# Optimization experiments

Measured on AMD Instinct MI355X. Metric: run time of the kernel, lower is better.

Reference implementation:

```python
import jax, jax.numpy as jnp
import numpy as np

D_MODEL, D_HEAD, N_HEAD = 1024, 64, 16
B, T1, T2 = 2, 2048, 2048


def setup_inputs() -> dict:
    key = jax.random.key(0)
    ks = jax.random.split(key, 8)
    s = 1.0 / np.sqrt(D_MODEL)
    return {
        "x": jax.random.normal(ks[0], (B, T1, D_MODEL), dtype=jnp.float32),
        "context": jax.random.normal(ks[1], (B, T2, D_MODEL), dtype=jnp.float32),
        "bias": jax.random.normal(ks[2], (T1, T2), dtype=jnp.float32),
        "W_q": jax.random.normal(ks[3], (D_MODEL, N_HEAD * D_HEAD), dtype=jnp.float32) * s,
        "W_k": jax.random.normal(ks[4], (D_MODEL, N_HEAD * D_HEAD), dtype=jnp.float32) * s,
        "W_v": jax.random.normal(ks[5], (D_MODEL, N_HEAD * D_HEAD), dtype=jnp.float32) * s,
        "W_out": jax.random.normal(ks[6], (N_HEAD * D_HEAD, D_MODEL), dtype=jnp.float32) * s,
        "b_out": jnp.zeros((D_MODEL,), dtype=jnp.float32),
    }


def reference(x, context, bias, W_q, W_k, W_v, W_out, b_out):
    Bq, T1_, _ = x.shape
    T2_ = context.shape[1]
    atten_scale = 1.0 / np.sqrt(D_HEAD)
    # fixed (non-trainable) per-head scale: 2^{-1}, ..., 2^{-n_head}
    head_scale = jnp.exp2(-jnp.arange(1, N_HEAD + 1, dtype=jnp.float32))

    # projections -> [B, H, T, d]
    q = (x @ W_q).reshape(Bq, T1_, N_HEAD, D_HEAD).transpose(0, 2, 1, 3)
    k = (context @ W_k).reshape(Bq, T2_, N_HEAD, D_HEAD).transpose(0, 2, 1, 3)
    v = (context @ W_v).reshape(Bq, T2_, N_HEAD, D_HEAD).transpose(0, 2, 1, 3)

    # scores: [B, H, T1, T2]
    scores = jnp.einsum("bhqd,bhkd->bhqk", q, k) * atten_scale
    scores = scores + bias[None, None, :, :] * head_scale[None, :, None, None]
    attn = jax.nn.softmax(scores, axis=-1)

    out = jnp.einsum("bhqk,bhkd->bqhd", attn, v).reshape(Bq, T1_, N_HEAD * D_HEAD)
    # dropout is identity in eval mode
    return out @ W_out + b_out
```

## Files before the change

### kernel.cpp

```cpp
#include <hip/hip_runtime.h>

typedef float  f32x4   __attribute__((ext_vector_type(4)));
typedef float  f32x16  __attribute__((ext_vector_type(16)));
typedef __bf16 bf16x8  __attribute__((ext_vector_type(8)));
typedef __bf16 bf16x4  __attribute__((ext_vector_type(4)));
typedef __bf16 bf16x2  __attribute__((ext_vector_type(2)));
typedef short  short8v __attribute__((ext_vector_type(8)));
typedef unsigned uint4v __attribute__((ext_vector_type(4)));

__device__ __forceinline__ short f2bf(float f) {
  unsigned u = __float_as_uint(f);
  unsigned r = (u + 0x7FFFu + ((u >> 16) & 1u)) >> 16;
  return (short)r;
}

__device__ __forceinline__ f32x4 mfma16(bf16x8 a, bf16x8 b, f32x4 c) {
  return __builtin_amdgcn_mfma_f32_16x16x32_bf16(a, b, c, 0, 0, 0);
}
__device__ __forceinline__ f32x16 mfma32(bf16x8 a, bf16x8 b, f32x16 c) {
  return __builtin_amdgcn_mfma_f32_32x32x16_bf16(a, b, c, 0, 0, 0);
}

__device__ __forceinline__ void gload16(const void* g, void* l) {
  __builtin_amdgcn_global_load_lds(
      (const __attribute__((address_space(1))) unsigned int*)g,
      (__attribute__((address_space(3))) unsigned int*)l,
      16, 0, 0);
}

__device__ __forceinline__ bf16x8 p_exchange(const unsigned* pk, int a, int hi) {
  unsigned y1 = hi ? pk[4 * a + 0] : pk[4 * a + 2];
  unsigned z1 = __shfl_xor(y1, 32);
  unsigned y2 = hi ? pk[4 * a + 1] : pk[4 * a + 3];
  unsigned z2 = __shfl_xor(y2, 32);
  unsigned w0 = hi ? z1 : pk[4 * a + 0];
  unsigned w1 = hi ? z2 : pk[4 * a + 1];
  unsigned w2 = hi ? pk[4 * a + 2] : z1;
  unsigned w3 = hi ? pk[4 * a + 3] : z2;
  uint4v q4 = {w0, w1, w2, w3};
  return __builtin_bit_cast(bf16x8, q4);
}


__global__ __launch_bounds__(256) void cvt_copy(const float* __restrict__ in,
                                                short* __restrict__ out, int n4) {
  int i = blockIdx.x * blockDim.x + threadIdx.x;
  int stride = gridDim.x * blockDim.x;
  for (; i < n4; i += stride) {
    float4 v = *(const float4*)&in[i * 4];
    short4 o;
    o.x = f2bf(v.x); o.y = f2bf(v.y); o.z = f2bf(v.z); o.w = f2bf(v.w);
    *(short4*)&out[i * 4] = o;
  }
}

__global__ __launch_bounds__(256) void cvt_transpose4(const float* __restrict__ W0,
                                                      const float* __restrict__ W1,
                                                      const float* __restrict__ W2,
                                                      const float* __restrict__ W3,
                                                      short* __restrict__ T0,
                                                      short* __restrict__ T1,
                                                      short* __restrict__ T2,
                                                      short* __restrict__ T3) {
  __shared__ short t_s[64][72];
  int z = blockIdx.z;
  const float* W = (z == 0) ? W0 : (z == 1) ? W1 : (z == 2) ? W2 : W3;
  short* Wt = (z == 0) ? T0 : (z == 1) ? T1 : (z == 2) ? T2 : T3;
  int k0 = blockIdx.y * 64, n0 = blockIdx.x * 64;
  int tid = threadIdx.x;
#pragma unroll
  for (int i = 0; i < 4; i++) {
    int idx = i * 256 + tid;
    int r = idx >> 4, cg = idx & 15;
    float4 v = *(const float4*)&W[(k0 + r) * 1024 + n0 + cg * 4];
    t_s[cg * 4 + 0][r] = f2bf(v.x);
    t_s[cg * 4 + 1][r] = f2bf(v.y);
    t_s[cg * 4 + 2][r] = f2bf(v.z);
    t_s[cg * 4 + 3][r] = f2bf(v.w);
  }
  __syncthreads();
#pragma unroll
  for (int i = 0; i < 2; i++) {
    int idx = i * 256 + tid;
    int r = idx >> 3, cg = idx & 7;
    short8v val = *(short8v*)&t_s[r][cg * 8];
    *(short8v*)&Wt[(n0 + r) * 1024 + k0 + cg * 8] = val;
  }
}

template <int EPI>
__global__ __launch_bounds__(256, 4) void gemm_bf16(const short* __restrict__ A,
                                                    const short* __restrict__ Bt,
                                                    void* __restrict__ out,
                                                    void* __restrict__ out2,
                                                    const float* __restrict__ bout) {
  constexpr int KD = 1024;
  constexpr int NB = (EPI == 3) ? 32 : 16;
  __shared__ short a_s[64][64];
  __shared__ short b_s[64][64];
  int tid = threadIdx.x, w = tid >> 6, lane = tid & 63;
  int g = lane >> 4, c16 = lane & 15;
  int hsw = c16 & 7;

  int lin = blockIdx.x + NB * blockIdx.y;
  int wk = (lin & 7) * (NB * 8) + (lin >> 3);
  int c0 = (wk & (NB - 1)) * 64, r0 = (wk / NB) * 64;

  int wr = (w >> 1) * 32, wc = (w & 1) * 32;
  f32x4 acc[2][2] = {};

  for (int kt = 0; kt < KD / 64; ++kt) {
    int k0 = kt * 64;
    __syncthreads();
#pragma unroll
    for (int i = 0; i < 2; i++) {
      int cb = i * 256 + w * 64;
      int c = cb + lane;
      int row = c >> 3, kg = c & 7;
      int sw = (kg ^ (row & 7)) * 8;
      gload16(A + (r0 + row) * KD + k0 + sw, (char*)a_s + cb * 16);
      gload16(Bt + (c0 + row) * KD + k0 + sw, (char*)b_s + cb * 16);
    }
    __syncthreads();
#pragma unroll
    for (int kk = 0; kk < 2; kk++) {
      bf16x8 af[2], bf[2];
      int sl0 = ((4 * kk + g) ^ hsw) * 8;
#pragma unroll
      for (int m = 0; m < 2; m++) af[m] = *(const bf16x8*)&a_s[wr + m * 16 + c16][sl0];
#pragma unroll
      for (int n = 0; n < 2; n++) bf[n] = *(const bf16x8*)&b_s[wc + n * 16 + c16][sl0];
#pragma unroll
      for (int m = 0; m < 2; m++)
#pragma unroll
        for (int n = 0; n < 2; n++) acc[m][n] = mfma16(af[m], bf[n], acc[m][n]);
    }
  }

#pragma unroll
  for (int m = 0; m < 2; m++)
#pragma unroll
    for (int n = 0; n < 2; n++)
#pragma unroll
      for (int r = 0; r < 4; r++) {
        int row = r0 + wr + m * 16 + g * 4 + r;
        int col = c0 + wc + n * 16 + c16;
        float v = acc[m][n][r];
        int b = row >> 11, t = row & 2047;
        if (EPI == 2) {
          ((float*)out)[row * 1024 + col] = v + bout[col];
        } else if (EPI == 0) {
          int h = col >> 6, d = col & 63;
          ((short*)out)[(((b * 16 + h) * 2048) + t) * 64 + d] = f2bf(v);
        } else {
          if (col < 1024) {
            int h = col >> 6, d = col & 63;
            ((short*)out)[(((b * 16 + h) * 2048) + t) * 64 + d] = f2bf(v);
          } else {
            int cv = col - 1024;
            int h = cv >> 6, d = cv & 63;
            ((short*)out2)[(((b * 16 + h) * 64) + d) * 2048 + t] = f2bf(v);
          }
        }
      }
}

__global__ __launch_bounds__(256, 4) void flash_attn(const short* __restrict__ Qg,
                                                     const short* __restrict__ Kg,
                                                     const short* __restrict__ Vtg,
                                                     const short* __restrict__ biasb,
                                                     short* __restrict__ Og) {
  __shared__ short k_s[2][64][64];
  __shared__ short v_s[2][64][64];

  int tid = threadIdx.x, w = tid >> 6, lane = tid & 63;
  int hi = lane >> 5, ll = lane & 31;
  int l7 = ll & 7;

  int lin = blockIdx.x + 16 * (blockIdx.y + 16 * blockIdx.z);
  int qi = (lin & 7) | (((lin >> 8) & 1) << 3);
  int h = (lin >> 3) & 15;
  int b = (lin >> 7) & 1;
  int qb = qi * 128;

  const short* Qh = Qg + (size_t)(b * 16 + h) * 2048 * 64;
  const short* Kh = Kg + (size_t)(b * 16 + h) * 2048 * 64;
  const short* Vh = Vtg + (size_t)(b * 16 + h) * 64 * 2048;

  const float C1 = 0.125f * 1.44269504f;
  const float C2 = exp2f(-(float)(h + 1)) * 1.44269504f;

  int qrow = qb + w * 32 + ll;
  const short* bp = biasb + (size_t)qrow * 2048 + 4 * hi;

#pragma unroll
  for (int i = 0; i < 2; i++) {
    int cb = i * 256 + w * 64;
    int c = cb + lane;
    int row = c >> 3, t8 = c & 7, sw = (t8 ^ (row & 7)) * 8;
    gload16(Kh + row * 64 + sw, (char*)&k_s[0][0][0] + cb * 16);
    gload16(Vh + row * 2048 + sw, (char*)&v_s[0][0][0] + cb * 16);
  }
  bf16x8 qf[4];
#pragma unroll
  for (int dm = 0; dm < 4; dm++)
    qf[dm] = *(const bf16x8*)(Qh + (size_t)qrow * 64 + dm * 16 + hi * 8);
  asm volatile("" ::: "memory");

  float l_run = 0.f;
  f32x16 o_acc[2] = {};

  for (int kt = 0; kt < 32; ++kt) {
    int cur = kt & 1;
    bf16x4 bv0[4];
#pragma unroll
    for (int u = 0; u < 4; u++)
      bv0[u] = *(const bf16x4*)(bp + kt * 64 + u * 8);

    if (kt < 31) {
      const short* Ks = Kh + (size_t)(kt + 1) * 64 * 64;
      const short* Vs = Vh + (kt + 1) * 64;
#pragma unroll
      for (int i = 0; i < 2; i++) {
        int cb = i * 256 + w * 64;
        int c = cb + lane;
        int row = c >> 3, t8 = c & 7, sw = (t8 ^ (row & 7)) * 8;
        gload16(Ks + row * 64 + sw, (char*)&k_s[cur ^ 1][0][0] + cb * 16);
        gload16(Vs + row * 2048 + sw, (char*)&v_s[cur ^ 1][0][0] + cb * 16);
      }
    }
    asm volatile("s_waitcnt vmcnt(8)" ::: "memory");
    __builtin_amdgcn_s_barrier();

    f32x16 sacc = {};
    __builtin_amdgcn_s_setprio(1);
#pragma unroll
    for (int dm = 0; dm < 4; dm++) {
      const short* kr = &k_s[cur][ll][((2 * dm + hi) ^ l7) * 8];
      sacc = mfma32(*(const bf16x8*)kr, qf[dm], sacc);
    }
    __builtin_amdgcn_s_setprio(0);

    float lp = 0.f;
    unsigned pk[8];
#pragma unroll
    for (int i = 0; i < 8; i++) {
      float b0 = (float)bv0[i >> 1][2 * (i & 1)];
      float b1 = (float)bv0[i >> 1][2 * (i & 1) + 1];
      float p0 = exp2f(sacc[2 * i] * C1 + b0 * C2);
      float p1 = exp2f(sacc[2 * i + 1] * C1 + b1 * C2);
      lp += p0 + p1;
      bf16x2 pp = {(__bf16)p0, (__bf16)p1};
      pk[i] = __builtin_bit_cast(unsigned, pp);
    }
    l_run += lp;

    bf16x4 bv1[4];
#pragma unroll
    for (int u = 0; u < 4; u++)
      bv1[u] = *(const bf16x4*)(bp + kt * 64 + 32 + u * 8);

    __builtin_amdgcn_s_setprio(1);
#pragma unroll
    for (int a = 0; a < 2; a++) {
      bf16x8 PA = p_exchange(pk, a, hi);
#pragma unroll
      for (int dt = 0; dt < 2; dt++) {
        const short* vr = &v_s[cur][dt * 32 + ll][((2 * a + hi) ^ l7) * 8];
        o_acc[dt] = mfma32(PA, *(const bf16x8*)vr, o_acc[dt]);
      }
    }
    __builtin_amdgcn_s_setprio(0);
    asm volatile("" ::: "memory");

    f32x16 sacc1 = {};
    __builtin_amdgcn_s_setprio(1);
#pragma unroll
    for (int dm = 0; dm < 4; dm++) {
      const short* kr = &k_s[cur][32 + ll][((2 * dm + hi) ^ l7) * 8];
      sacc1 = mfma32(*(const bf16x8*)kr, qf[dm], sacc1);
    }
    __builtin_amdgcn_s_setprio(0);

    float lp1 = 0.f;
#pragma unroll
    for (int i = 0; i < 8; i++) {
      float b0 = (float)bv1[i >> 1][2 * (i & 1)];
      float b1 = (float)bv1[i >> 1][2 * (i & 1) + 1];
      float p0 = exp2f(sacc1[2 * i] * C1 + b0 * C2);
      float p1 = exp2f(sacc1[2 * i + 1] * C1 + b1 * C2);
      lp1 += p0 + p1;
      bf16x2 pp = {(__bf16)p0, (__bf16)p1};
      pk[i] = __builtin_bit_cast(unsigned, pp);
    }
    l_run += lp1;

    __builtin_amdgcn_s_setprio(1);
#pragma unroll
    for (int a = 0; a < 2; a++) {
      bf16x8 PA = p_exchange(pk, a, hi);
#pragma unroll
      for (int dt = 0; dt < 2; dt++) {
        const short* vr = &v_s[cur][dt * 32 + ll][((4 + 2 * a + hi) ^ l7) * 8];
        o_acc[dt] = mfma32(PA, *(const bf16x8*)vr, o_acc[dt]);
      }
    }
    __builtin_amdgcn_s_setprio(0);
    __builtin_amdgcn_s_barrier();
  }

  l_run += __shfl_xor(l_run, 32);
  float invl = 1.f / l_run;

#pragma unroll
  for (int r = 0; r < 16; r++) {
    int q = (r & 3) + 8 * (r >> 2) + 4 * hi;
    float iv = __shfl(invl, q);
    int tg = qb + w * 32 + q;
#pragma unroll
    for (int dt = 0; dt < 2; dt++) {
      Og[(size_t)(b * 2048 + tg) * 1024 + h * 64 + dt * 32 + ll] =
          f2bf(o_acc[dt][r] * iv);
    }
  }
}

extern "C" void kernel_launch(void* const* d_in, const int* in_sizes, int n_in,
                              void* d_out, int out_size, void* d_ws, size_t ws_size,
                              hipStream_t stream) {
  const float* x    = (const float*)d_in[0];
  const float* ctx  = (const float*)d_in[1];
  const float* bias = (const float*)d_in[2];
  const float* Wq   = (const float*)d_in[3];
  const float* Wk   = (const float*)d_in[4];
  const float* Wv   = (const float*)d_in[5];
  const float* Wo   = (const float*)d_in[6];
  const float* bo   = (const float*)d_in[7];
  float* out = (float*)d_out;

  char* ws = (char*)d_ws;
  short* x_bf = (short*)(ws + 0);
  short* c_bf = (short*)(ws + 8388608);
  short* wq_t = (short*)(ws + 16777216);
  short* wk_t = (short*)(ws + 18874368);
  short* wv_t = (short*)(ws + 20971520);
  short* wo_t = (short*)(ws + 23068672);
  short* q_ws = (short*)(ws + 25165824);
  short* k_ws = (short*)(ws + 33554432);
  short* v_ws = (short*)(ws + 41943040);
  short* o_ws = (short*)(ws + 50331648);
  short* bias_bf = x_bf;

  cvt_copy<<<1024, 256, 0, stream>>>(x, x_bf, 1048576);
  cvt_copy<<<1024, 256, 0, stream>>>(ctx, c_bf, 1048576);
  dim3 tg(16, 16, 4);
  cvt_transpose4<<<tg, 256, 0, stream>>>(Wq, Wk, Wv, Wo, wq_t, wk_t, wv_t, wo_t);

  dim3 gq(16, 64);
  gemm_bf16<0><<<gq, 256, 0, stream>>>(x_bf, wq_t, q_ws, nullptr, nullptr);
  dim3 gkv(32, 64);
  gemm_bf16<3><<<gkv, 256, 0, stream>>>(c_bf, wk_t, k_ws, v_ws, nullptr);

  cvt_copy<<<1024, 256, 0, stream>>>(bias, bias_bf, 1048576);

  dim3 fg(16, 16, 2);
  flash_attn<<<fg, 256, 0, stream>>>(q_ws, k_ws, v_ws, bias_bf, o_ws);

  gemm_bf16<2><<<gq, 256, 0, stream>>>(o_ws, wo_t, out, nullptr, bo);
}
```

Before: 188.2 us.

## Split key tiles across two wave groups per block and merge partial outputs

Doubles the flash-attention block to 512 threads, with two groups of four waves each processing alternating 64-key tiles for the same 128 query rows. Both tiles are staged per iteration in double-buffered LDS, which halves the serial loop length per wave. Partial O accumulators and row sums are reduced through shared memory at the end. This raises wave count per query block to hide latency, at the cost of more LDS per block, an extra reduction step, and a changed block-to-work mapping.

After: 181.5 us. 3.5% less time.

```diff
diff --git a/kernel.cpp b/kernel.cpp
--- a/kernel.cpp
+++ b/kernel.cpp
@@ -165,23 +165,23 @@
       }
 }
 
-__global__ __launch_bounds__(256, 4) void flash_attn(const short* __restrict__ Qg,
+__global__ __launch_bounds__(512, 4) void flash_attn(const short* __restrict__ Qg,
                                                      const short* __restrict__ Kg,
                                                      const short* __restrict__ Vtg,
                                                      const short* __restrict__ biasb,
                                                      short* __restrict__ Og) {
-  __shared__ short k_s[2][64][64];
-  __shared__ short v_s[2][64][64];
+  __shared__ short k_s[2][2][64][64];
+  __shared__ short v_s[2][2][64][64];
 
   int tid = threadIdx.x, w = tid >> 6, lane = tid & 63;
-  int hi = lane >> 5, ll = lane & 31;
-  int l7 = ll & 7;
+  int gid = w >> 2, w4 = w & 3;
+  int hi = lane >> 5, ll = lane & 31, l7 = ll & 7;
 
   int lin = blockIdx.x + 16 * (blockIdx.y + 16 * blockIdx.z);
-  int qi = (lin & 7) | (((lin >> 8) & 1) << 3);
-  int h = (lin >> 3) & 15;
-  int b = (lin >> 7) & 1;
-  int qb = qi * 128;
+  int wk = (lin & 7) * 64 + (lin >> 3);
+  int qb = (wk & 15) * 128;
+  int h = (wk >> 4) & 15;
+  int b = wk >> 8;
 
   const short* Qh = Qg + (size_t)(b * 16 + h) * 2048 * 64;
   const short* Kh = Kg + (size_t)(b * 16 + h) * 2048 * 64;
@@ -190,16 +190,21 @@
   const float C1 = 0.125f * 1.44269504f;
   const float C2 = exp2f(-(float)(h + 1)) * 1.44269504f;
 
-  int qrow = qb + w * 32 + ll;
+  int qrow = qb + w4 * 32 + ll;
   const short* bp = biasb + (size_t)qrow * 2048 + 4 * hi;
 
-#pragma unroll
-  for (int i = 0; i < 2; i++) {
-    int cb = i * 256 + w * 64;
-    int c = cb + lane;
-    int row = c >> 3, t8 = c & 7, sw = (t8 ^ (row & 7)) * 8;
-    gload16(Kh + row * 64 + sw, (char*)&k_s[0][0][0] + cb * 16);
-    gload16(Vh + row * 2048 + sw, (char*)&v_s[0][0][0] + cb * 16);
+  int srow = tid >> 3, st8 = tid & 7;
+  int ssw = (st8 ^ (srow & 7)) * 8;
+
+  {
+    char* kd0 = (char*)&k_s[0][0][0][0] + w * 64 * 16;
+    char* vd0 = (char*)&v_s[0][0][0][0] + w * 64 * 16;
+    char* kd1 = (char*)&k_s[0][1][0][0] + w * 64 * 16;
+    char* vd1 = (char*)&v_s[0][1][0][0] + w * 64 * 16;
+    gload16(Kh + srow * 64 + ssw, kd0);
+    gload16(Vh + srow * 2048 + ssw, vd0);
+    gload16(Kh + 64 * 64 + srow * 64 + ssw, kd1);
+    gload16(Vh + srow * 2048 + 64 + ssw, vd1);
   }
   bf16x8 qf[4];
 #pragma unroll
@@ -210,33 +215,35 @@
   float l_run = 0.f;
   f32x16 o_acc[2] = {};
 
-  for (int kt = 0; kt < 32; ++kt) {
-    int cur = kt & 1;
+  for (int r = 0; r < 16; ++r) {
+    int cur = r & 1;
+    int kt = 2 * r + gid;
     bf16x4 bv0[4];
 #pragma unroll
     for (int u = 0; u < 4; u++)
       bv0[u] = *(const bf16x4*)(bp + kt * 64 + u * 8);
 
-    if (kt < 31) {
-      const short* Ks = Kh + (size_t)(kt + 1) * 64 * 64;
-      const short* Vs = Vh + (kt + 1) * 64;
-#pragma unroll
-      for (int i = 0; i < 2; i++) {
-        int cb = i * 256 + w * 64;
-        int c = cb + lane;
-        int row = c >> 3, t8 = c & 7, sw = (t8 ^ (row & 7)) * 8;
-        gload16(Ks + row * 64 + sw, (char*)&k_s[cur ^ 1][0][0] + cb * 16);
-        gload16(Vs + row * 2048 + sw, (char*)&v_s[cur ^ 1][0][0] + cb * 16);
-      }
-    }
-    asm volatile("s_waitcnt vmcnt(8)" ::: "memory");
+    if (r < 15) {
+      int tA = 2 * r + 2;
+      char* kdA = (char*)&k_s[cur ^ 1][0][0][0] + w * 64 * 16;
+      char* vdA = (char*)&v_s[cur ^ 1][0][0][0] + w * 64 * 16;
+      char* kdB = (char*)&k_s[cur ^ 1][1][0][0] + w * 64 * 16;
+      char* vdB = (char*)&v_s[cur ^ 1][1][0][0] + w * 64 * 16;
+      gload16(Kh + (size_t)tA * 4096 + srow * 64 + ssw, kdA);
+      gload16(Vh + srow * 2048 + tA * 64 + ssw, vdA);
+      gload16(Kh + (size_t)(tA + 1) * 4096 + srow * 64 + ssw, kdB);
+      gload16(Vh + srow * 2048 + (tA + 1) * 64 + ssw, vdB);
+      asm volatile("s_waitcnt vmcnt(8)" ::: "memory");
+    } else {
+      asm volatile("s_waitcnt vmcnt(4)" ::: "memory");
+    }
     __builtin_amdgcn_s_barrier();
 
     f32x16 sacc = {};
     __builtin_amdgcn_s_setprio(1);
 #pragma unroll
     for (int dm = 0; dm < 4; dm++) {
-      const short* kr = &k_s[cur][ll][((2 * dm + hi) ^ l7) * 8];
+      const short* kr = &k_s[cur][gid][ll][((2 * dm + hi) ^ l7) * 8];
       sacc = mfma32(*(const bf16x8*)kr, qf[dm], sacc);
     }
     __builtin_amdgcn_s_setprio(0);
@@ -266,7 +273,7 @@
       bf16x8 PA = p_exchange(pk, a, hi);
 #pragma unroll
       for (int dt = 0; dt < 2; dt++) {
-        const short* vr = &v_s[cur][dt * 32 + ll][((2 * a + hi) ^ l7) * 8];
+        const short* vr = &v_s[cur][gid][dt * 32 + ll][((2 * a + hi) ^ l7) * 8];
         o_acc[dt] = mfma32(PA, *(const bf16x8*)vr, o_acc[dt]);
       }
     }
@@ -277,7 +284,7 @@
     __builtin_amdgcn_s_setprio(1);
 #pragma unroll
     for (int dm = 0; dm < 4; dm++) {
-      const short* kr = &k_s[cur][32 + ll][((2 * dm + hi) ^ l7) * 8];
+      const short* kr = &k_s[cur][gid][32 + ll][((2 * dm + hi) ^ l7) * 8];
       sacc1 = mfma32(*(const bf16x8*)kr, qf[dm], sacc1);
     }
     __builtin_amdgcn_s_setprio(0);
@@ -301,7 +308,7 @@
       bf16x8 PA = p_exchange(pk, a, hi);
 #pragma unroll
       for (int dt = 0; dt < 2; dt++) {
-        const short* vr = &v_s[cur][dt * 32 + ll][((4 + 2 * a + hi) ^ l7) * 8];
+        const short* vr = &v_s[cur][gid][dt * 32 + ll][((4 + 2 * a + hi) ^ l7) * 8];
         o_acc[dt] = mfma32(PA, *(const bf16x8*)vr, o_acc[dt]);
       }
     }
@@ -310,17 +317,31 @@
   }
 
   l_run += __shfl_xor(l_run, 32);
-  float invl = 1.f / l_run;
-
-#pragma unroll
-  for (int r = 0; r < 16; r++) {
-    int q = (r & 3) + 8 * (r >> 2) + 4 * hi;
-    float iv = __shfl(invl, q);
-    int tg = qb + w * 32 + q;
-#pragma unroll
-    for (int dt = 0; dt < 2; dt++) {
-      Og[(size_t)(b * 2048 + tg) * 1024 + h * 64 + dt * 32 + ll] =
-          f2bf(o_acc[dt][r] * iv);
+  float* ox = (float*)&k_s[0][0][0][0];
+  float* lx = (float*)&v_s[0][0][0][0];
+  if (gid == 1) {
+#pragma unroll
+    for (int k = 0; k < 32; k++)
+      ox[(w4 * 32 + k) * 64 + lane] = o_acc[k >> 4][k & 15];
+    if (lane < 32) lx[w4 * 32 + lane] = l_run;
+  }
+  __syncthreads();
+  if (gid == 0) {
+    float invl = 1.f / (l_run + lx[w4 * 32 + ll]);
+#pragma unroll
+    for (int k = 0; k < 32; k++)
+      o_acc[k >> 4][k & 15] += ox[(w4 * 32 + k) * 64 + lane];
+
+#pragma unroll
+    for (int r = 0; r < 16; r++) {
+      int q = (r & 3) + 8 * (r >> 2) + 4 * hi;
+      float iv = __shfl(invl, q);
+      int tg = qb + w4 * 32 + q;
+#pragma unroll
+      for (int dt = 0; dt < 2; dt++) {
+        Og[(size_t)(b * 2048 + tg) * 1024 + h * 64 + dt * 32 + ll] =
+            f2bf(o_acc[dt][r] * iv);
+      }
     }
   }
 }
@@ -364,7 +385,7 @@
   cvt_copy<<<1024, 256, 0, stream>>>(bias, bias_bf, 1048576);
 
   dim3 fg(16, 16, 2);
-  flash_attn<<<fg, 256, 0, stream>>>(q_ws, k_ws, v_ws, bias_bf, o_ws);
+  flash_attn<<<fg, 512, 0, stream>>>(q_ws, k_ws, v_ws, bias_bf, o_ws);
 
   gemm_bf16<2><<<gq, 256, 0, stream>>>(o_ws, wo_t, out, nullptr, bo);
 }
```
